# Kernel optimization log

Hardware: AMD Instinct MI355X
Metric: run time of the kernel (lower is better)

Reference implementation:

```python
import jax, jax.numpy as jnp
import numpy as np

N = 1000        # genomes
S = 32          # samples
M = 2_000_000   # total genes
K = 100_000     # sequences (contigs)


def setup_inputs() -> dict:
    key = jax.random.key(0)
    k1, k2, k3, k4, k5 = jax.random.split(key, 5)
    A = jax.random.normal(k1, (N, S), dtype=jnp.float32)          # log-abundance
    B = jax.random.uniform(k2, (N, S), dtype=jnp.float32)         # log-PTR in [0,1]
    pos = jax.random.uniform(k3, (M,), dtype=jnp.float32)         # gene position in [0,1]
    genome_idx = jax.random.randint(k4, (M,), 0, N)               # one-hot column of `members`
    seq_idx = jax.random.randint(k5, (M,), 0, K)                  # row of `gene_to_seq`
    return {"A": A, "B": B, "pos": pos, "genome_idx": genome_idx, "seq_idx": seq_idx}


def reference(A, B, pos, genome_idx, seq_idx):
    # G = members @ A + 1 - dists @ B  ==  A[g] + 1 - pos * B[g] per gene  -> [M, S]
    G = A[genome_idx] + 1.0 - pos[:, None] * B[genome_idx]
    # E @ exp(G): sum exp(G) over genes belonging to each sequence -> [K, S]
    return jax.ops.segment_sum(jnp.exp(G), seq_idx, num_segments=K)
```

## Files before the change

### kernel.cpp

```cpp
#include <hip/hip_runtime.h>
#include <hip/hip_bf16.h>


#define CHUNK 8192
#define NBMAX 1024
#define CAPLG 12
#define CAP   (1 << CAPLG)
#define SCAP  3072

__device__ inline float fast_exp2(float x) {
    float r;
    asm("v_exp_f32 %0, %1" : "=v"(r) : "v"(x));
    return r;
}

__global__ __launch_bounds__(256) void prep_kernel(
    const float* __restrict__ A, const float* __restrict__ B,
    unsigned* __restrict__ AB2p, int* __restrict__ gcur, int NS)
{
    const int i = blockIdx.x * 256 + threadIdx.x;
    if (i < NBMAX) gcur[i] = 0;
    if (i >= NS) return;
    const float a2 = (A[i] + 1.0f) * 1.44269504f;
    const float b2 = B[i] * (1.44269504f / 32768.0f);
    const _Float16 ha = (_Float16)a2;
    const unsigned short ua = __builtin_bit_cast(unsigned short, ha);
    unsigned bb = __float_as_uint(b2);
    bb = (bb + 0x7FFFu + ((bb >> 16) & 1u)) & 0xFFFF0000u;
    AB2p[i] = (unsigned)ua | bb;
}

__global__ __launch_bounds__(1024) void partition_kernel(
    const float* __restrict__ pos, const int* __restrict__ gidx,
    const int* __restrict__ sidx, int* __restrict__ gcur,
    unsigned* __restrict__ payload, int M, int NB)
{
    __shared__ int h[NBMAX];
    __shared__ int pfx[NBMAX];
    __shared__ int dbase[NBMAX];
    __shared__ int wsum[16];
    __shared__ unsigned stg_p[CHUNK];
    __shared__ unsigned short stg_b[CHUNK];
    const int t = threadIdx.x, blk = blockIdx.x;
    const int i0 = blk * CHUNK;
    const int n = min(CHUNK, M - i0);

    h[t] = 0;
    __syncthreads();

    unsigned pl[8];
    int bb[8], rk[8];
#pragma unroll
    for (int u = 0; u < 8; u++) {
        const int j = t + u * 1024;
        rk[u] = -1;
        if (j < n) {
            const int sx = sidx[i0 + j];
            const int b = sx >> 7;
            const float p = pos[i0 + j];
            int q = (int)fmaf(p, 32768.0f, 0.5f);
            q = min(q, 32767);
            pl[u] = (unsigned)(sx & 127)
                  | ((unsigned)gidx[i0 + j] << 7)
                  | ((unsigned)q << 17);
            bb[u] = b;
            rk[u] = atomicAdd(&h[b], 1);
        }
    }
    __syncthreads();

    {
        const int v = h[t];
        int incl = v;
#pragma unroll
        for (int d = 1; d < 64; d <<= 1) {
            const int x = __shfl_up(incl, d);
            if ((t & 63) >= d) incl += x;
        }
        if ((t & 63) == 63) wsum[t >> 6] = incl;
        __syncthreads();
        if (t < 16) {
            const int wv = wsum[t];
            int winc = wv;
#pragma unroll
            for (int d = 1; d < 16; d <<= 1) {
                const int x = __shfl_up(winc, d, 16);
                if (t >= d) winc += x;
            }
            wsum[t] = winc - wv;
        }
        __syncthreads();
        pfx[t] = wsum[t >> 6] + incl - v;
    }
    __syncthreads();

#pragma unroll
    for (int u = 0; u < 8; u++)
        if (rk[u] >= 0) {
            const int d = pfx[bb[u]] + rk[u];
            stg_p[d] = pl[u];
            stg_b[d] = (unsigned short)bb[u];
        }
    __syncthreads();

    if (t < NB) {
        const int hc = h[t];
        int dst = t << CAPLG;
        if (hc > 0) dst += atomicAdd(&gcur[t], hc);
        dbase[t] = dst;
    }
    __syncthreads();

    for (int tt = t; tt < n; tt += 1024) {
        const int b = stg_b[tt];
        const int r = dbase[b] + (tt - pfx[b]);
        if ((r >> CAPLG) == b) payload[r] = stg_p[tt];
    }
}

__global__ __launch_bounds__(512) void fused_reduce_kernel(
    const unsigned* __restrict__ AB2p, const unsigned* __restrict__ payload,
    const int* __restrict__ gcur, float* __restrict__ out, int K)
{
    __shared__ unsigned sorted[SCAP + 8];
    __shared__ int h[64];
    __shared__ int pfx[64];
    const int t = threadIdx.x;
    const int bkt = blockIdx.x >> 1;
    const int sp  = blockIdx.x & 1;
    const int g4  = (t >> 4) & 3;
    const int l16 = t & 15;
    const unsigned lane8 = (unsigned)(l16 << 3);
    const int wv = t >> 6;
    const int start = bkt << CAPLG;
    const int n = min(gcur[bkt], CAP);

    if (t < 64) h[t] = 0;
    __syncthreads();

    unsigned r[8];
    int rk[8];
#pragma unroll
    for (int u = 0; u < 8; u++) {
        const int idx = t + u * 512;
        rk[u] = -1;
        if (idx < n) {
            const unsigned w = payload[start + idx];
            if ((int)((w >> 6) & 1u) == sp) {
                r[u] = w;
                rk[u] = atomicAdd(&h[w & 63], 1);
            }
        }
    }
    __syncthreads();

    if (t < 64) {
        const int v = h[t];
        int incl = v;
#pragma unroll
        for (int d = 1; d < 64; d <<= 1) {
            const int x = __shfl_up(incl, d);
            if (t >= d) incl += x;
        }
        pfx[t] = incl - v;
    }
    __syncthreads();

#pragma unroll
    for (int u = 0; u < 8; u++)
        if (rk[u] >= 0) {
            const int d = pfx[r[u] & 63] + rk[u];
            if (d < SCAP) sorted[d] = r[u];
        }
    __syncthreads();

#define GPROC(gi, A0, A1)                                                     \
    {                                                                         \
        const unsigned w = sorted[gi];                                        \
        const bool valid = (gi) < e;                                          \
        const unsigned voff = (w & 0x1FF80u) | lane8;                         \
        const uint2 ab = *(const uint2*)((const char*)AB2p + voff);           \
        const float qf = (float)(w >> 17);                                    \
        float fa0, fa1;                                                       \
        asm("v_cvt_f32_f16 %0, %1" : "=v"(fa0) : "v"(ab.x));                  \
        asm("v_cvt_f32_f16 %0, %1" : "=v"(fa1) : "v"(ab.y));                  \
        float x0 = fmaf(-qf, __int_as_float(ab.x & 0xFFFF0000u), fa0);        \
        float x1 = fmaf(-qf, __int_as_float(ab.y & 0xFFFF0000u), fa1);        \
        x0 = valid ? x0 : -2000.0f;                                           \
        x1 = valid ? x1 : -2000.0f;                                           \
        A0 += fast_exp2(x0);                                                  \
        A1 += fast_exp2(x1);                                                  \
    }

    const int seqbase = (bkt << 7) + (sp << 6) + (wv << 3);
    for (int q = 0; q < 8; q++) {
        const int ls = (wv << 3) + q;
        const int i0 = pfx[ls];
        const int e = min(i0 + h[ls], SCAP);
        float a0 = 0.0f, a1 = 0.0f, b0 = 0.0f, b1 = 0.0f;
        int i = i0;
        for (; i + 4 < e; i += 8) {
            GPROC(i + g4, a0, a1);
            GPROC(i + 4 + g4, b0, b1);
        }
        for (; i < e; i += 4)
            GPROC(i + g4, a0, a1);
        float acc0 = a0 + b0, acc1 = a1 + b1;
        acc0 += __shfl_xor(acc0, 16);
        acc1 += __shfl_xor(acc1, 16);
        acc0 += __shfl_xor(acc0, 32);
        acc1 += __shfl_xor(acc1, 32);
        const int seq = seqbase + q;
        if ((t & 48) == 0 && seq < K)
            *(float2*)&out[(seq << 5) + (l16 << 1)] = make_float2(acc0, acc1);
    }
#undef GPROC
}

__global__ __launch_bounds__(256) void scatter_exp_fallback(
    const float* __restrict__ A, const float* __restrict__ B,
    const float* __restrict__ pos, const int* __restrict__ gidx,
    const int* __restrict__ sidx, float* __restrict__ out, int M)
{
    const int lane = threadIdx.x & 31;
    int group = (int)((blockIdx.x * blockDim.x + threadIdx.x) >> 5);
    const int stride = (int)((gridDim.x * blockDim.x) >> 5);
    for (int g = group; g < M; g += stride) {
        const int gi = gidx[g];
        const int si = sidx[g];
        const float p = pos[g];
        const float a = A[(gi << 5) + lane];
        const float b = B[(gi << 5) + lane];
        atomicAdd(&out[(si << 5) + lane], __expf(fmaf(-p, b, a + 1.0f)));
    }
}

extern "C" void kernel_launch(void* const* d_in, const int* in_sizes, int n_in,
                              void* d_out, int out_size, void* d_ws, size_t ws_size,
                              hipStream_t stream)
{
    const float* A    = (const float*)d_in[0];
    const float* B    = (const float*)d_in[1];
    const float* pos  = (const float*)d_in[2];
    const int*   gidx = (const int*)d_in[3];
    const int*   sidx = (const int*)d_in[4];
    float*       out  = (float*)d_out;

    const int M  = in_sizes[2];
    const int NS = in_sizes[0];
    const int N  = NS / 32;
    const int K  = out_size / 32;
    const int NB = (K + 127) >> 7;
    const int NBLK = (M + CHUNK - 1) / CHUNK;

    char* ws = (char*)d_ws;
    size_t off = 0;
    int* gcur = (int*)(ws + off);       off += (size_t)NBMAX * sizeof(int);
    off = (off + 255) & ~(size_t)255;
    unsigned* AB2p = (unsigned*)(ws + off); off += (size_t)N * 32 * sizeof(unsigned);
    off = (off + 255) & ~(size_t)255;
    unsigned* payload = (unsigned*)(ws + off);
    const size_t need = off + ((size_t)NB << CAPLG) * sizeof(unsigned);

    const bool packable = (NB <= NBMAX) && (K <= NBMAX * 128) && (N <= 1024)
                       && (M / (NB > 0 ? NB : 1) <= CAP / 4 * 3);
    if (!packable || ws_size < need) {
        hipMemsetAsync(d_out, 0, (size_t)out_size * sizeof(float), stream);
        scatter_exp_fallback<<<8192, 256, 0, stream>>>(A, B, pos, gidx, sidx, out, M);
        return;
    }

    const int prep_grid = (max(NS, NBMAX) + 255) / 256;
    prep_kernel     <<<prep_grid, 256, 0, stream>>>(A, B, AB2p, gcur, NS);
    partition_kernel<<<NBLK, 1024, 0, stream>>>(pos, gidx, sidx, gcur, payload, M, NB);
    fused_reduce_kernel<<<NB * 2, 512, 0, stream>>>(AB2p, payload, gcur, out, K);
}
```

Baseline: 57.27 us.

## Replace global atomic bucket scatter with per-block descriptor table and gather in reducer

The partition kernel no longer scatters payloads into global buckets through atomic cursors. Each block now writes its locally sorted chunk contiguously and records a per-bin offset and count descriptor covering 2048 bins of 64 sequences. Each reduce block reads the descriptors for its bin across all partition blocks, gathers those runs into shared memory, then does the per-sequence local sort and exp-sum as before. This removes the global atomics, the bucket overflow capacity and the half-split reduce blocks, at the cost of a descriptor table write and many small strided gathers per reduce block. Segments that exceed RCAP are silently truncated.

After: 58.25 us. No clear change (+1.7%).

```diff
diff --git a/kernel.cpp b/kernel.cpp
--- a/kernel.cpp
+++ b/kernel.cpp
@@ -3,10 +3,9 @@
 
 
 #define CHUNK 8192
-#define NBMAX 1024
-#define CAPLG 12
-#define CAP   (1 << CAPLG)
-#define SCAP  3072
+#define NBIN  2048
+#define NBLKMAX 256
+#define RCAP  2048
 
 __device__ inline float fast_exp2(float x) {
     float r;
@@ -16,10 +15,9 @@
 
 __global__ __launch_bounds__(256) void prep_kernel(
     const float* __restrict__ A, const float* __restrict__ B,
-    unsigned* __restrict__ AB2p, int* __restrict__ gcur, int NS)
+    unsigned* __restrict__ AB2p, int NS)
 {
     const int i = blockIdx.x * 256 + threadIdx.x;
-    if (i < NBMAX) gcur[i] = 0;
     if (i >= NS) return;
     const float a2 = (A[i] + 1.0f) * 1.44269504f;
     const float b2 = B[i] * (1.44269504f / 32768.0f);
@@ -32,20 +30,18 @@
 
 __global__ __launch_bounds__(1024) void partition_kernel(
     const float* __restrict__ pos, const int* __restrict__ gidx,
-    const int* __restrict__ sidx, int* __restrict__ gcur,
-    unsigned* __restrict__ payload, int M, int NB)
-{
-    __shared__ int h[NBMAX];
-    __shared__ int pfx[NBMAX];
-    __shared__ int dbase[NBMAX];
+    const int* __restrict__ sidx, unsigned* __restrict__ payload,
+    unsigned* __restrict__ desc, int M, int NB2)
+{
+    __shared__ int h[NBIN];
+    __shared__ int pfx[NBIN];
     __shared__ int wsum[16];
     __shared__ unsigned stg_p[CHUNK];
-    __shared__ unsigned short stg_b[CHUNK];
     const int t = threadIdx.x, blk = blockIdx.x;
     const int i0 = blk * CHUNK;
     const int n = min(CHUNK, M - i0);
 
-    h[t] = 0;
+    h[t] = 0; h[t + 1024] = 0;
     __syncthreads();
 
     unsigned pl[8];
@@ -56,22 +52,22 @@
         rk[u] = -1;
         if (j < n) {
             const int sx = sidx[i0 + j];
-            const int b = sx >> 7;
             const float p = pos[i0 + j];
             int q = (int)fmaf(p, 32768.0f, 0.5f);
             q = min(q, 32767);
-            pl[u] = (unsigned)(sx & 127)
+            pl[u] = (unsigned)(sx & 63)
                   | ((unsigned)gidx[i0 + j] << 7)
                   | ((unsigned)q << 17);
-            bb[u] = b;
-            rk[u] = atomicAdd(&h[b], 1);
+            bb[u] = sx >> 6;
+            rk[u] = atomicAdd(&h[bb[u]], 1);
         }
     }
     __syncthreads();
 
     {
-        const int v = h[t];
-        int incl = v;
+        const int v0 = h[2 * t], v1 = h[2 * t + 1];
+        const int s = v0 + v1;
+        int incl = s;
 #pragma unroll
         for (int d = 1; d < 64; d <<= 1) {
             const int x = __shfl_up(incl, d);
@@ -90,66 +86,87 @@
             wsum[t] = winc - wv;
         }
         __syncthreads();
-        pfx[t] = wsum[t >> 6] + incl - v;
+        const int ex = wsum[t >> 6] + incl - s;
+        pfx[2 * t] = ex;
+        pfx[2 * t + 1] = ex + v0;
     }
     __syncthreads();
 
 #pragma unroll
     for (int u = 0; u < 8; u++)
-        if (rk[u] >= 0) {
-            const int d = pfx[bb[u]] + rk[u];
-            stg_p[d] = pl[u];
-            stg_b[d] = (unsigned short)bb[u];
-        }
-    __syncthreads();
-
-    if (t < NB) {
-        const int hc = h[t];
-        int dst = t << CAPLG;
-        if (hc > 0) dst += atomicAdd(&gcur[t], hc);
-        dbase[t] = dst;
-    }
-    __syncthreads();
-
-    for (int tt = t; tt < n; tt += 1024) {
-        const int b = stg_b[tt];
-        const int r = dbase[b] + (tt - pfx[b]);
-        if ((r >> CAPLG) == b) payload[r] = stg_p[tt];
-    }
+        if (rk[u] >= 0) stg_p[pfx[bb[u]] + rk[u]] = pl[u];
+    __syncthreads();
+
+    for (int b = t; b < NB2; b += 1024)
+        desc[(size_t)blk * NBIN + b] = (unsigned)pfx[b] | ((unsigned)h[b] << 16);
+
+    for (int tt = t; tt < n; tt += 1024)
+        payload[i0 + tt] = stg_p[tt];
 }
 
 __global__ __launch_bounds__(512) void fused_reduce_kernel(
     const unsigned* __restrict__ AB2p, const unsigned* __restrict__ payload,
-    const int* __restrict__ gcur, float* __restrict__ out, int K)
-{
-    __shared__ unsigned sorted[SCAP + 8];
-    __shared__ int h[64];
-    __shared__ int pfx[64];
-    const int t = threadIdx.x;
-    const int bkt = blockIdx.x >> 1;
-    const int sp  = blockIdx.x & 1;
-    const int g4  = (t >> 4) & 3;
+    const unsigned* __restrict__ desc, float* __restrict__ out,
+    int K, int NBLK)
+{
+    __shared__ unsigned stg[RCAP];
+    __shared__ unsigned sorted[RCAP + 8];
+    __shared__ int rc[NBLKMAX], ro[NBLKMAX], rs[NBLKMAX];
+    __shared__ int h[64], pfx[64];
+    const int t = threadIdx.x, bkt = blockIdx.x;
     const int l16 = t & 15;
+    const int g4 = (t >> 4) & 3;
+    const int wv = t >> 6;
+    const int grp16 = t >> 4;
     const unsigned lane8 = (unsigned)(l16 << 3);
-    const int wv = t >> 6;
-    const int start = bkt << CAPLG;
-    const int n = min(gcur[bkt], CAP);
 
     if (t < 64) h[t] = 0;
-    __syncthreads();
-
-    unsigned r[8];
-    int rk[8];
-#pragma unroll
-    for (int u = 0; u < 8; u++) {
+    if (t < NBLKMAX) { rc[t] = 0; ro[t] = 0; }
+    __syncthreads();
+    if (t < NBLK) {
+        const unsigned d = desc[(size_t)t * NBIN + bkt];
+        ro[t] = (int)(d & 0xFFFFu);
+        rc[t] = (int)(d >> 16);
+    }
+    __syncthreads();
+
+    if (t < 64) {
+        int v[4], s = 0;
+#pragma unroll
+        for (int j = 0; j < 4; j++) { v[j] = rc[4 * t + j]; s += v[j]; }
+        int incl = s;
+#pragma unroll
+        for (int d = 1; d < 64; d <<= 1) {
+            const int x = __shfl_up(incl, d);
+            if (t >= d) incl += x;
+        }
+        int ex = incl - s;
+#pragma unroll
+        for (int j = 0; j < 4; j++) { rs[4 * t + j] = ex; ex += v[j]; }
+    }
+    __syncthreads();
+
+    for (int rb = grp16; rb < NBLK; rb += 32) {
+        const int cnt = rc[rb], base = rs[rb];
+        const unsigned src = (unsigned)rb * CHUNK + (unsigned)ro[rb];
+        for (int i = l16; i < cnt; i += 16) {
+            const int d = base + i;
+            if (d < RCAP) stg[d] = payload[src + i];
+        }
+    }
+    __syncthreads();
+
+    const int nt = min(rs[NBLKMAX - 1] + rc[NBLKMAX - 1], RCAP);
+
+    unsigned r[4];
+    int rk[4];
+#pragma unroll
+    for (int u = 0; u < 4; u++) {
         const int idx = t + u * 512;
         rk[u] = -1;
-        if (idx < n) {
-            const unsigned w = payload[start + idx];
-            if ((int)((w >> 6) & 1u) == sp) {
-                r[u] = w;
-                rk[u] = atomicAdd(&h[w & 63], 1);
-            }
+        if (idx < nt) {
+            r[u] = stg[idx];
+            rk[u] = atomicAdd(&h[r[u] & 63], 1);
         }
     }
     __syncthreads();
@@ -167,11 +184,8 @@
     __syncthreads();
 
 #pragma unroll
-    for (int u = 0; u < 8; u++)
-        if (rk[u] >= 0) {
-            const int d = pfx[r[u] & 63] + rk[u];
-            if (d < SCAP) sorted[d] = r[u];
-        }
+    for (int u = 0; u < 4; u++)
+        if (rk[u] >= 0) sorted[pfx[r[u] & 63] + rk[u]] = r[u];
     __syncthreads();
 
 #define GPROC(gi, A0, A1)                                                     \
@@ -192,13 +206,13 @@
         A1 += fast_exp2(x1);                                                  \
     }
 
-    const int seqbase = (bkt << 7) + (sp << 6) + (wv << 3);
+    const int seqbase = (bkt << 6) + (wv << 3);
     for (int q = 0; q < 8; q++) {
         const int ls = (wv << 3) + q;
-        const int i0 = pfx[ls];
-        const int e = min(i0 + h[ls], SCAP);
+        const int s0 = pfx[ls];
+        const int e = s0 + h[ls];
         float a0 = 0.0f, a1 = 0.0f, b0 = 0.0f, b1 = 0.0f;
-        int i = i0;
+        int i = s0;
         for (; i + 4 < e; i += 8) {
             GPROC(i + g4, a0, a1);
             GPROC(i + 4 + g4, b0, b1);
@@ -250,28 +264,27 @@
     const int NS = in_sizes[0];
     const int N  = NS / 32;
     const int K  = out_size / 32;
-    const int NB = (K + 127) >> 7;
+    const int NB2 = (K + 63) >> 6;
     const int NBLK = (M + CHUNK - 1) / CHUNK;
 
     char* ws = (char*)d_ws;
     size_t off = 0;
-    int* gcur = (int*)(ws + off);       off += (size_t)NBMAX * sizeof(int);
-    off = (off + 255) & ~(size_t)255;
     unsigned* AB2p = (unsigned*)(ws + off); off += (size_t)N * 32 * sizeof(unsigned);
     off = (off + 255) & ~(size_t)255;
+    unsigned* desc = (unsigned*)(ws + off); off += (size_t)NBLK * NBIN * sizeof(unsigned);
+    off = (off + 255) & ~(size_t)255;
     unsigned* payload = (unsigned*)(ws + off);
-    const size_t need = off + ((size_t)NB << CAPLG) * sizeof(unsigned);
-
-    const bool packable = (NB <= NBMAX) && (K <= NBMAX * 128) && (N <= 1024)
-                       && (M / (NB > 0 ? NB : 1) <= CAP / 4 * 3);
+    const size_t need = off + (size_t)NBLK * CHUNK * sizeof(unsigned);
+
+    const bool packable = (NB2 <= NBIN) && (NBLK <= NBLKMAX) && (N <= 1024)
+                       && (K <= NBIN * 64);
     if (!packable || ws_size < need) {
         hipMemsetAsync(d_out, 0, (size_t)out_size * sizeof(float), stream);
         scatter_exp_fallback<<<8192, 256, 0, stream>>>(A, B, pos, gidx, sidx, out, M);
         return;
     }
 
-    const int prep_grid = (max(NS, NBMAX) + 255) / 256;
-    prep_kernel     <<<prep_grid, 256, 0, stream>>>(A, B, AB2p, gcur, NS);
-    partition_kernel<<<NBLK, 1024, 0, stream>>>(pos, gidx, sidx, gcur, payload, M, NB);
-    fused_reduce_kernel<<<NB * 2, 512, 0, stream>>>(AB2p, payload, gcur, out, K);
-}
+    prep_kernel     <<<(NS + 255) / 256, 256, 0, stream>>>(A, B, AB2p, NS);
+    partition_kernel<<<NBLK, 1024, 0, stream>>>(pos, gidx, sidx, payload, desc, M, NB2);
+    fused_reduce_kernel<<<NB2, 512, 0, stream>>>(AB2p, payload, desc, out, K, NBLK);
+}
```

## Double partition chunk size and scatter per bucket with 16-lane groups

Applied to the files above, without the earlier changes.

Doubles the per-block chunk in the partition kernel to 16384 elements, halving the block count and the global atomics on bucket cursors. It drops the separate per-element bucket-id staging array by packing bucket and rank into one register, and removes one barrier. The global write-out now walks buckets with 16-lane groups instead of iterating elements. This makes contiguous writes per bucket, but costs more registers and shared memory per block and may leave lanes idle on small buckets.

After: 59.78 us. 1.04x slower.

```diff
diff --git a/kernel.cpp b/kernel.cpp
--- a/kernel.cpp
+++ b/kernel.cpp
@@ -2,7 +2,7 @@
 #include <hip/hip_bf16.h>
 
 
-#define CHUNK 8192
+#define CHUNK 16384
 #define NBMAX 1024
 #define CAPLG 12
 #define CAP   (1 << CAPLG)
@@ -40,20 +40,20 @@
     __shared__ int dbase[NBMAX];
     __shared__ int wsum[16];
     __shared__ unsigned stg_p[CHUNK];
-    __shared__ unsigned short stg_b[CHUNK];
     const int t = threadIdx.x, blk = blockIdx.x;
     const int i0 = blk * CHUNK;
     const int n = min(CHUNK, M - i0);
+    const int l16 = t & 15, grp16 = t >> 4;
 
     h[t] = 0;
     __syncthreads();
 
-    unsigned pl[8];
-    int bb[8], rk[8];
-#pragma unroll
-    for (int u = 0; u < 8; u++) {
+    unsigned pl[16];
+    int rkbb[16];
+#pragma unroll
+    for (int u = 0; u < 16; u++) {
         const int j = t + u * 1024;
-        rk[u] = -1;
+        rkbb[u] = -1;
         if (j < n) {
             const int sx = sidx[i0 + j];
             const int b = sx >> 7;
@@ -63,8 +63,7 @@
             pl[u] = (unsigned)(sx & 127)
                   | ((unsigned)gidx[i0 + j] << 7)
                   | ((unsigned)q << 17);
-            bb[u] = b;
-            rk[u] = atomicAdd(&h[b], 1);
+            rkbb[u] = (b << 18) | atomicAdd(&h[b], 1);
         }
     }
     __syncthreads();
@@ -95,13 +94,9 @@
     __syncthreads();
 
 #pragma unroll
-    for (int u = 0; u < 8; u++)
-        if (rk[u] >= 0) {
-            const int d = pfx[bb[u]] + rk[u];
-            stg_p[d] = pl[u];
-            stg_b[d] = (unsigned short)bb[u];
-        }
-    __syncthreads();
+    for (int u = 0; u < 16; u++)
+        if (rkbb[u] >= 0)
+            stg_p[pfx[rkbb[u] >> 18] + (rkbb[u] & 0x3FFFF)] = pl[u];
 
     if (t < NB) {
         const int hc = h[t];
@@ -111,10 +106,15 @@
     }
     __syncthreads();
 
-    for (int tt = t; tt < n; tt += 1024) {
-        const int b = stg_b[tt];
-        const int r = dbase[b] + (tt - pfx[b]);
-        if ((r >> CAPLG) == b) payload[r] = stg_p[tt];
+    for (int b = grp16; b < NB; b += 64) {
+        const int cnt = h[b];
+        if (cnt == 0) continue;
+        const int src = pfx[b];
+        const int dst = dbase[b];
+        for (int i = l16; i < cnt; i += 16) {
+            const int rr = dst + i;
+            if ((rr >> CAPLG) == b) payload[rr] = stg_p[src + i];
+        }
     }
 }
 
@@ -146,7 +146,7 @@
         rk[u] = -1;
         if (idx < n) {
             const unsigned w = payload[start + idx];
-            if ((int)((w >> 6) & 1u) == sp) {
+            if (((w >> 6) & 1u) == (unsigned)sp) {
                 r[u] = w;
                 rk[u] = atomicAdd(&h[w & 63], 1);
             }
```
